# Optimization experiments

Hardware: AMD Instinct MI355X
Metric: run time of the kernel (lower is better)

The kernel has to match this reference:

```python
import jax, jax.numpy as jnp
import numpy as np

N = 100000   # nodes
E = 3200000  # edges (avg degree 32)
IN = 128     # in_channels
H = 128      # hidden_channels
G = 512      # graphs in batch


def setup_inputs() -> dict:
    key = jax.random.key(0)
    ks = jax.random.split(key, 8)
    x = jax.random.normal(ks[0], (N, IN), dtype=jnp.float32)
    edge_index = jax.random.randint(ks[1], (2, E), 0, N, dtype=jnp.int64)
    batch = jnp.sort(jax.random.randint(ks[2], (N,), 0, G, dtype=jnp.int64))
    s_in = 1.0 / np.sqrt(IN)
    s_h = 1.0 / np.sqrt(H)
    W1 = jax.random.normal(ks[3], (IN, H), dtype=jnp.float32) * s_in
    b1 = jnp.zeros((H,), dtype=jnp.float32)
    W2 = jax.random.normal(ks[4], (H, H), dtype=jnp.float32) * s_h
    b2 = jnp.zeros((H,), dtype=jnp.float32)
    Wc = jax.random.normal(ks[5], (H, 1), dtype=jnp.float32) * s_h
    bc = jnp.zeros((1,), dtype=jnp.float32)
    return {"x": x, "edge_index": edge_index, "batch": batch,
            "W1": W1, "b1": b1, "W2": W2, "b2": b2, "Wc": Wc, "bc": bc}


def _gcn_conv(x, W, b, src, dst, n):
    # PyG GCNConv: x' = D^{-1/2} (A+I) D^{-1/2} X W + b  (self-loops already in src/dst)
    h = x @ W                                      # [n, H] small GEMM
    ones = jnp.ones(src.shape[0], dtype=h.dtype)
    deg = jax.ops.segment_sum(ones, dst, num_segments=n)
    dinv = jnp.where(deg > 0, jax.lax.rsqrt(deg), 0.0)
    norm = dinv[src] * dinv[dst]                   # [E+n]
    msgs = h[src] * norm[:, None]                  # gather + scale (memory-bound)
    return jax.ops.segment_sum(msgs, dst, num_segments=n) + b


def reference(x, edge_index, batch, W1, b1, W2, b2, Wc, bc):
    n = x.shape[0]
    loop = jnp.arange(n, dtype=edge_index.dtype)
    src = jnp.concatenate([edge_index[0], loop])   # add self-loops
    dst = jnp.concatenate([edge_index[1], loop])
    h = jax.nn.relu(_gcn_conv(x, W1, b1, src, dst, n))
    h = jax.nn.relu(_gcn_conv(h, W2, b2, src, dst, n))
    # global_mean_pool: segment mean over graph ids
    counts = jax.ops.segment_sum(jnp.ones(n, dtype=h.dtype), batch, num_segments=G)
    sums = jax.ops.segment_sum(h, batch, num_segments=G)
    pooled = sums / jnp.maximum(counts, 1.0)[:, None]   # [G, H]
    return jax.nn.sigmoid(pooled @ Wc + bc)             # [G, 1]
```

## Files before the change

kernel.cpp:

```cpp
#include <hip/hip_runtime.h>

typedef unsigned short ushort_t;
typedef unsigned int uint_t;
typedef unsigned char u8_t;

typedef __bf16 bf16x8 __attribute__((ext_vector_type(8)));
typedef float f32x4 __attribute__((ext_vector_type(4)));
typedef uint_t uint32x4 __attribute__((ext_vector_type(4)));
typedef uint_t uint32x2 __attribute__((ext_vector_type(2)));
typedef _Float16 h2 __attribute__((ext_vector_type(2)));

#define EPB 20480
#define NSH 7
#define CAP 6144

__device__ __forceinline__ float b2f(ushort_t u) {
    union { uint_t ui; float f; } c; c.ui = ((uint_t)u) << 16; return c.f;
}
__device__ __forceinline__ ushort_t f2b(float f) {
    union { float f; uint_t ui; } c; c.f = f;
    uint_t u = c.ui;
    uint_t r = (u + 0x7fffu + ((u >> 16) & 1u)) >> 16;
    return (ushort_t)r;
}
__device__ __forceinline__ u8_t f2e5(float x) {
    ushort_t h = __builtin_bit_cast(ushort_t, (_Float16)x);
    uint_t r = ((uint_t)h + 0x7Fu + ((h >> 8) & 1u)) >> 8;
    return (u8_t)r;
}
__device__ __forceinline__ void upk_add(uint_t d, h2* acc) {
    uint_t A = __builtin_amdgcn_perm(0u, d, 0x010C000Cu);
    uint_t B = __builtin_amdgcn_perm(0u, d, 0x030C020Cu);
    acc[0] += __builtin_bit_cast(h2, A);
    acc[1] += __builtin_bit_cast(h2, B);
}

__global__ __launch_bounds__(256) void p1_hist(const int* __restrict__ dst,
                                               int* __restrict__ H,
                                               const float* __restrict__ W1,
                                               const float* __restrict__ W2,
                                               ushort_t* __restrict__ W1t,
                                               ushort_t* __restrict__ W2t,
                                               int E, int NBLK, int B) {
    int t = threadIdx.x, c = blockIdx.x;
    if (c >= NBLK) {
        int idx = (c - NBLK) * 256 + t;
        int sel = idx >> 14;
        int i = idx & 16383;
        int k = i >> 7, nn = i & 127;
        const float* S = sel ? W2 : W1;
        ushort_t* D = sel ? W2t : W1t;
        D[nn * 128 + k] = f2b(S[k * 128 + nn]);
        return;
    }
    __shared__ int hist[1024];
    for (int b = t; b < 1024; b += 256) hist[b] = 0;
    __syncthreads();
    int base = c * EPB;
    int lim = min(E - base, EPB);
    for (int i = t; i < lim; i += 256)
        atomicAdd(&hist[dst[base + i] >> NSH], 1);
    __syncthreads();
    for (int b = t; b < B; b += 256) H[b * NBLK + c] = hist[b];
}

__global__ __launch_bounds__(256) void reduce256(const int* __restrict__ in,
                                                 int* __restrict__ bsums, int n) {
    __shared__ int s[256];
    int t = threadIdx.x, g = blockIdx.x * 256 + t;
    s[t] = (g < n) ? in[g] : 0;
    __syncthreads();
    for (int o = 128; o > 0; o >>= 1) {
        if (t < o) s[t] += s[t + o];
        __syncthreads();
    }
    if (t == 0) bsums[blockIdx.x] = s[0];
}

__global__ __launch_bounds__(512) void scan_small(const int* __restrict__ in,
                                                  int* __restrict__ outEx, int n) {
    __shared__ int s[512];
    int t = threadIdx.x;
    int v = (t < n) ? in[t] : 0;
    s[t] = v;
    __syncthreads();
    for (int o = 1; o < 512; o <<= 1) {
        int x = 0;
        if (t >= o) x = s[t - o];
        __syncthreads();
        s[t] += x;
        __syncthreads();
    }
    if (t < n) outEx[t] = s[t] - v;
}

__global__ __launch_bounds__(256) void scan256ex(const int* __restrict__ in,
                                                 const int* __restrict__ boffs,
                                                 int* __restrict__ outEx, int n) {
    __shared__ int s[256];
    int t = threadIdx.x, g = blockIdx.x * 256 + t;
    int v = (g < n) ? in[g] : 0;
    s[t] = v;
    __syncthreads();
    for (int o = 1; o < 256; o <<= 1) {
        int x = 0;
        if (t >= o) x = s[t - o];
        __syncthreads();
        s[t] += x;
        __syncthreads();
    }
    if (g < n) outEx[g] = boffs[blockIdx.x] + s[t] - v;
}

__global__ __launch_bounds__(256) void p3_scatter(const int* __restrict__ src,
                                                  const int* __restrict__ dst,
                                                  const int* __restrict__ Hex,
                                                  uint_t* __restrict__ packed,
                                                  int E, int NBLK, int B) {
    __shared__ int offsL[1024];
    __shared__ int cur[1024];
    int t = threadIdx.x, c = blockIdx.x;
    for (int b = t; b < B; b += 256) {
        offsL[b] = Hex[b * NBLK + c];
        cur[b] = 0;
    }
    __syncthreads();
    int base = c * EPB;
    int lim = min(E - base, EPB);
    for (int i = t; i < lim; i += 256) {
        int d = dst[base + i];
        int s = src[base + i];
        int b = d >> NSH;
        int r = atomicAdd(&cur[b], 1);
        packed[offsL[b] + r] = ((uint_t)s << NSH) | (uint_t)(d & 127);
    }
}

__global__ __launch_bounds__(256) void p4_build(const uint_t* __restrict__ packed,
                                                const int* __restrict__ Hex,
                                                int* __restrict__ adj,
                                                int* __restrict__ offs,
                                                float* __restrict__ dinv,
                                                int E, int N, int NBLK, int B) {
    __shared__ uint_t ebuf[CAP];
    __shared__ uint_t sbuf[CAP];
    __shared__ int hist[1024];
    __shared__ int hbase[1024];
    __shared__ int psum[256];
    __shared__ int dcnt[128], loc[128], cur[128];
    int t = threadIdx.x, b = blockIdx.x;
    int bs = Hex[b * NBLK];
    int be = (b + 1 < B) ? Hex[(b + 1) * NBLK] : E;
    int m = be - bs;
    for (int i = t; i < 1024; i += 256) hist[i] = 0;
    if (t < 128) dcnt[t] = 0;
    __syncthreads();
    bool fits = (m <= CAP);
    for (int i = t; i < m; i += 256) {
        uint_t p = packed[bs + i];
        if (fits) ebuf[i] = p;
        atomicAdd(&dcnt[p & 127], 1);
        atomicAdd(&hist[p >> (2 * NSH)], 1);
    }
    __syncthreads();
    int v0 = hist[4 * t], v1 = hist[4 * t + 1], v2 = hist[4 * t + 2], v3 = hist[4 * t + 3];
    int tot = v0 + v1 + v2 + v3;
    psum[t] = tot;
    __syncthreads();
    for (int o = 1; o < 256; o <<= 1) {
        int x = 0;
        if (t >= o) x = psum[t - o];
        __syncthreads();
        psum[t] += x;
        __syncthreads();
    }
    int base = psum[t] - tot;
    hbase[4 * t]     = base;
    hbase[4 * t + 1] = base + v0;
    hbase[4 * t + 2] = base + v0 + v1;
    hbase[4 * t + 3] = base + v0 + v1 + v2;
    if (t < 128) loc[t] = dcnt[t];
    __syncthreads();
    for (int o = 1; o < 128; o <<= 1) {
        int x = 0;
        if (t < 128 && t >= o) x = loc[t - o];
        __syncthreads();
        if (t < 128) loc[t] += x;
        __syncthreads();
    }
    if (t < 128) {
        int ex = loc[t] - dcnt[t];
        int node = b * 128 + t;
        if (node < N) {
            offs[node] = bs + ex;
            dinv[node] = rsqrtf((float)(dcnt[t] + 1));
        }
        loc[t] = ex;
        cur[t] = 0;
    }
    if (b == B - 1 && t == 0) offs[N] = E;
    __syncthreads();
    if (fits) {
        for (int i = t; i < m; i += 256) {
            uint_t p = ebuf[i];
            int r = atomicAdd(&hbase[p >> (2 * NSH)], 1);
            sbuf[r] = p;
        }
        __syncthreads();
        for (int i = t; i < m; i += 256) {
            uint_t p = sbuf[i];
            int l = p & 127;
            int r = atomicAdd(&cur[l], 1);
            adj[bs + loc[l] + r] = (int)(p >> NSH);
        }
    } else {
        for (int i = t; i < m; i += 256) {
            uint_t p = packed[bs + i];
            int l = p & 127;
            int r = atomicAdd(&cur[l], 1);
            adj[bs + loc[l] + r] = (int)(p >> NSH);
        }
    }
}

__global__ __launch_bounds__(256, 4) void gemm_scale(const ushort_t* __restrict__ Xin,
                                                     const ushort_t* __restrict__ Wt,
                                                     const float* __restrict__ dinv,
                                                     u8_t* __restrict__ Hout8, int n) {
    __shared__ ushort_t lds[128 * 136];
    int tid = threadIdx.x;
    for (int i = tid; i < 128 * 16; i += 256) {
        int r = i >> 4, c8 = (i & 15) << 3;
        *(uint32x4*)(lds + r * 136 + c8) = *(const uint32x4*)(Wt + r * 128 + c8);
    }
    __syncthreads();
    int lane = tid & 63, wave = tid >> 6;
    int m = lane & 15, q = lane >> 4;
    int row0 = blockIdx.x * 64 + wave * 16;
    int ar = row0 + m;
    if (ar > n - 1) ar = n - 1;
    bf16x8 a[4];
#pragma unroll
    for (int ks = 0; ks < 4; ++ks)
        a[ks] = __builtin_bit_cast(bf16x8,
            *(const uint32x4*)(Xin + (size_t)ar * 128 + ks * 32 + q * 8));
    f32x4 acc[8];
    f32x4 zero = {0.f, 0.f, 0.f, 0.f};
#pragma unroll
    for (int nt = 0; nt < 8; ++nt) acc[nt] = zero;
#pragma unroll
    for (int nt = 0; nt < 8; ++nt) {
#pragma unroll
        for (int ks = 0; ks < 4; ++ks) {
            bf16x8 b = __builtin_bit_cast(bf16x8,
                *(const uint32x4*)(lds + (nt * 16 + m) * 136 + ks * 32 + q * 8));
            acc[nt] = __builtin_amdgcn_mfma_f32_16x16x32_bf16(a[ks], b, acc[nt], 0, 0, 0);
        }
    }
    float dv[4];
#pragma unroll
    for (int r = 0; r < 4; ++r) {
        int gr = row0 + q * 4 + r;
        dv[r] = (gr < n) ? dinv[gr] : 0.f;
    }
#pragma unroll
    for (int nt = 0; nt < 8; ++nt) {
#pragma unroll
        for (int r = 0; r < 4; ++r) {
            int gr = row0 + q * 4 + r;
            if (gr < n)
                Hout8[(size_t)gr * 128 + nt * 16 + m] = f2e5(acc[nt][r] * dv[r]);
        }
    }
}

__global__ __launch_bounds__(256, 4) void gemm_scale_f32(const float* __restrict__ Xf,
                                                         const ushort_t* __restrict__ Wt,
                                                         const float* __restrict__ dinv,
                                                         u8_t* __restrict__ Hout8, int n) {
    __shared__ ushort_t lds[128 * 136];
    int tid = threadIdx.x;
    for (int i = tid; i < 128 * 16; i += 256) {
        int r = i >> 4, c8 = (i & 15) << 3;
        *(uint32x4*)(lds + r * 136 + c8) = *(const uint32x4*)(Wt + r * 128 + c8);
    }
    __syncthreads();
    int lane = tid & 63, wave = tid >> 6;
    int m = lane & 15, q = lane >> 4;
    int row0 = blockIdx.x * 64 + wave * 16;
    int ar = row0 + m;
    if (ar > n - 1) ar = n - 1;
    bf16x8 a[4];
#pragma unroll
    for (int ks = 0; ks < 4; ++ks) {
        const float* p = Xf + (size_t)ar * 128 + ks * 32 + q * 8;
        f32x4 lo = *(const f32x4*)p;
        f32x4 hi = *(const f32x4*)(p + 4);
        ushort_t t[8];
        t[0] = f2b(lo[0]); t[1] = f2b(lo[1]); t[2] = f2b(lo[2]); t[3] = f2b(lo[3]);
        t[4] = f2b(hi[0]); t[5] = f2b(hi[1]); t[6] = f2b(hi[2]); t[7] = f2b(hi[3]);
        a[ks] = __builtin_bit_cast(bf16x8, *(uint32x4*)t);
    }
    f32x4 acc[8];
    f32x4 zero = {0.f, 0.f, 0.f, 0.f};
#pragma unroll
    for (int nt = 0; nt < 8; ++nt) acc[nt] = zero;
#pragma unroll
    for (int nt = 0; nt < 8; ++nt) {
#pragma unroll
        for (int ks = 0; ks < 4; ++ks) {
            bf16x8 b = __builtin_bit_cast(bf16x8,
                *(const uint32x4*)(lds + (nt * 16 + m) * 136 + ks * 32 + q * 8));
            acc[nt] = __builtin_amdgcn_mfma_f32_16x16x32_bf16(a[ks], b, acc[nt], 0, 0, 0);
        }
    }
    float dv[4];
#pragma unroll
    for (int r = 0; r < 4; ++r) {
        int gr = row0 + q * 4 + r;
        dv[r] = (gr < n) ? dinv[gr] : 0.f;
    }
#pragma unroll
    for (int nt = 0; nt < 8; ++nt) {
#pragma unroll
        for (int r = 0; r < 4; ++r) {
            int gr = row0 + q * 4 + r;
            if (gr < n)
                Hout8[(size_t)gr * 128 + nt * 16 + m] = f2e5(acc[nt][r] * dv[r]);
        }
    }
}

__device__ __forceinline__ void agg_body(const u8_t* base8, const int* __restrict__ adj,
                                         int beg, int end, int g, h2* acc) {
    int e = beg;
    for (; e + 32 <= end; e += 32) {
        int s[8];
#pragma unroll
        for (int j = 0; j < 8; ++j) s[j] = adj[e + 4 * j + g];
        uint32x2 w[8];
#pragma unroll
        for (int j = 0; j < 8; ++j) w[j] = *(const uint32x2*)(base8 + (size_t)s[j] * 128);
#pragma unroll
        for (int j = 0; j < 8; ++j) {
            upk_add(w[j][0], acc);
            upk_add(w[j][1], acc + 2);
        }
    }
    for (; e + 8 <= end; e += 8) {
        int s0 = adj[e + g], s1 = adj[e + 4 + g];
        uint32x2 w0 = *(const uint32x2*)(base8 + (size_t)s0 * 128);
        uint32x2 w1 = *(const uint32x2*)(base8 + (size_t)s1 * 128);
        upk_add(w0[0], acc); upk_add(w0[1], acc + 2);
        upk_add(w1[0], acc); upk_add(w1[1], acc + 2);
    }
    for (; e < end; e += 4) {
        int idx = e + g;
        if (idx < end) {
            int s = adj[idx];
            uint32x2 w = *(const uint32x2*)(base8 + (size_t)s * 128);
            upk_add(w[0], acc);
            upk_add(w[1], acc + 2);
        }
    }
}

__global__ __launch_bounds__(256, 8) void agg_kernel(const u8_t* __restrict__ Hs8,
                                                     const int* __restrict__ adj,
                                                     const int* __restrict__ offs,
                                                     const float* __restrict__ dinv,
                                                     const float* __restrict__ bias,
                                                     ushort_t* __restrict__ Out, int n) {
    int node = blockIdx.x * 4 + (threadIdx.x >> 6);
    if (node >= n) return;
    int lane = threadIdx.x & 63;
    int g = lane >> 4;
    int l16 = lane & 15;
    int col = l16 * 8;
    const u8_t* base8 = Hs8 + col;
    const int beg = offs[node], end = offs[node + 1];
    h2 acc[4];
    h2 hz = {(_Float16)0.f, (_Float16)0.f};
#pragma unroll
    for (int k = 0; k < 4; ++k) acc[k] = hz;
    if (g == 0) {
        uint32x2 w = *(const uint32x2*)(base8 + (size_t)node * 128);
        upk_add(w[0], acc);
        upk_add(w[1], acc + 2);
    }
    agg_body(base8, adj, beg, end, g, acc);
#pragma unroll
    for (int k = 0; k < 4; ++k) {
        uint_t v = __builtin_bit_cast(uint_t, acc[k]);
        acc[k] += __builtin_bit_cast(h2, (uint_t)__shfl_xor(v, 16, 64));
        v = __builtin_bit_cast(uint_t, acc[k]);
        acc[k] += __builtin_bit_cast(h2, (uint_t)__shfl_xor(v, 32, 64));
    }
    if (g == 0) {
        float di = dinv[node];
        ushort_t o[8];
#pragma unroll
        for (int k = 0; k < 4; ++k) {
            float f0 = (float)acc[k][0];
            float f1 = (float)acc[k][1];
            o[2 * k]     = f2b(fmaxf(di * f0 + bias[col + 2 * k], 0.f));
            o[2 * k + 1] = f2b(fmaxf(di * f1 + bias[col + 2 * k + 1], 0.f));
        }
        *(uint32x4*)(Out + (size_t)node * 128 + col) = *(uint32x4*)o;
    }
}

__global__ __launch_bounds__(256, 8) void agg_pool_kernel(const u8_t* __restrict__ Hs8,
                                                          const int* __restrict__ adj,
                                                          const int* __restrict__ offs,
                                                          const float* __restrict__ dinv,
                                                          const float* __restrict__ bias,
                                                          const float* __restrict__ Wc,
                                                          float* __restrict__ Sout, int n) {
    int node = blockIdx.x * 4 + (threadIdx.x >> 6);
    if (node >= n) return;
    int lane = threadIdx.x & 63;
    int g = lane >> 4;
    int l16 = lane & 15;
    int col = l16 * 8;
    const u8_t* base8 = Hs8 + col;
    const int beg = offs[node], end = offs[node + 1];
    h2 acc[4];
    h2 hz = {(_Float16)0.f, (_Float16)0.f};
#pragma unroll
    for (int k = 0; k < 4; ++k) acc[k] = hz;
    if (g == 0) {
        uint32x2 w = *(const uint32x2*)(base8 + (size_t)node * 128);
        upk_add(w[0], acc);
        upk_add(w[1], acc + 2);
    }
    agg_body(base8, adj, beg, end, g, acc);
#pragma unroll
    for (int k = 0; k < 4; ++k) {
        uint_t v = __builtin_bit_cast(uint_t, acc[k]);
        acc[k] += __builtin_bit_cast(h2, (uint_t)__shfl_xor(v, 16, 64));
        v = __builtin_bit_cast(uint_t, acc[k]);
        acc[k] += __builtin_bit_cast(h2, (uint_t)__shfl_xor(v, 32, 64));
    }
    float local = 0.f;
    float di = dinv[node];
#pragma unroll
    for (int k = 0; k < 4; ++k) {
        float f0 = fmaxf(di * (float)acc[k][0] + bias[col + 2 * k], 0.f);
        float f1 = fmaxf(di * (float)acc[k][1] + bias[col + 2 * k + 1], 0.f);
        local += f0 * Wc[col + 2 * k] + f1 * Wc[col + 2 * k + 1];
    }
    local += __shfl_xor(local, 1, 64);
    local += __shfl_xor(local, 2, 64);
    local += __shfl_xor(local, 4, 64);
    local += __shfl_xor(local, 8, 64);
    if (lane == 0) Sout[node] = local;
}

__global__ __launch_bounds__(256) void pool2_kernel(const float* __restrict__ S,
                                                    const int* __restrict__ batch,
                                                    const float* __restrict__ bc,
                                                    float* __restrict__ out, int n) {
    int g = blockIdx.x;
    int t = threadIdx.x;
    int lo = 0, hi = n;
    while (lo < hi) { int mid = (lo + hi) >> 1; if (batch[mid] < g) lo = mid + 1; else hi = mid; }
    int start = lo;
    hi = n;
    while (lo < hi) { int mid = (lo + hi) >> 1; if (batch[mid] < g + 1) lo = mid + 1; else hi = mid; }
    int stop = lo;
    float s = 0.f;
    for (int i = start + t; i < stop; i += 256) s += S[i];
    __shared__ float red[256];
    red[t] = s;
    __syncthreads();
    for (int o = 128; o > 0; o >>= 1) {
        if (t < o) red[t] += red[t + o];
        __syncthreads();
    }
    if (t == 0) {
        int cg = stop - start;
        float z = red[0] / (float)(cg > 0 ? cg : 1) + bc[0];
        out[g] = 1.f / (1.f + expf(-z));
    }
}

extern "C" void kernel_launch(void* const* d_in, const int* in_sizes, int n_in,
                              void* d_out, int out_size, void* d_ws, size_t ws_size,
                              hipStream_t stream) {
    const float* X     = (const float*)d_in[0];
    const int* ei      = (const int*)d_in[1];
    const int* batch   = (const int*)d_in[2];
    const float* W1    = (const float*)d_in[3];
    const float* b1    = (const float*)d_in[4];
    const float* W2    = (const float*)d_in[5];
    const float* b2    = (const float*)d_in[6];
    const float* Wc    = (const float*)d_in[7];
    const float* bc    = (const float*)d_in[8];

    const int N = in_sizes[2];
    const int E = in_sizes[1] / 2;
    const int G = out_size;
    const int* srcv = ei;
    const int* dstv = ei + E;

    const int NBLK = (E + EPB - 1) / EPB;
    const int B    = (N + 127) >> NSH;
    const int n0   = B * NBLK;
    const int g1   = (n0 + 255) / 256;

    char* p = (char*)d_ws;
    auto alloc = [&](size_t bytes) -> void* {
        void* r = (void*)p;
        p += (bytes + 255) & ~(size_t)255;
        return r;
    };
    int* H         = (int*)alloc((size_t)n0 * 4);
    int* Hex       = (int*)alloc((size_t)n0 * 4);
    int* S1        = (int*)alloc((size_t)g1 * 4);
    int* S1ex      = (int*)alloc((size_t)g1 * 4);
    uint_t* packed = (uint_t*)alloc((size_t)E * 4);
    int* adj       = (int*)alloc((size_t)E * 4);
    int* offs      = (int*)alloc(((size_t)N + 1) * 4);
    float* dinv    = (float*)alloc((size_t)N * 4);
    ushort_t* W1t  = (ushort_t*)alloc(16384 * 2);
    ushort_t* W2t  = (ushort_t*)alloc(16384 * 2);
    u8_t* h8       = (u8_t*)alloc((size_t)N * 128);
    ushort_t* bufA = (ushort_t*)alloc((size_t)N * 128 * 2);
    float* Snode   = (float*)alloc((size_t)N * 4);

    p1_hist<<<NBLK + 128, 256, 0, stream>>>(dstv, H, W1, W2, W1t, W2t, E, NBLK, B);
    reduce256<<<g1, 256, 0, stream>>>(H, S1, n0);
    scan_small<<<1, 512, 0, stream>>>(S1, S1ex, g1);
    scan256ex<<<g1, 256, 0, stream>>>(H, S1ex, Hex, n0);
    p3_scatter<<<NBLK, 256, 0, stream>>>(srcv, dstv, Hex, packed, E, NBLK, B);
    p4_build<<<B, 256, 0, stream>>>(packed, Hex, adj, offs, dinv, E, N, NBLK, B);

    const int GB = (N + 63) / 64;
    const int AB = (N + 3) / 4;
    gemm_scale_f32<<<GB, 256, 0, stream>>>(X, W1t, dinv, h8, N);
    agg_kernel<<<AB, 256, 0, stream>>>(h8, adj, offs, dinv, b1, bufA, N);
    gemm_scale<<<GB, 256, 0, stream>>>(bufA, W2t, dinv, h8, N);
    agg_pool_kernel<<<AB, 256, 0, stream>>>(h8, adj, offs, dinv, b2, Wc, Snode, N);
    pool2_kernel<<<G, 256, 0, stream>>>(Snode, batch, bc, (float*)d_out, N);
}
```

Before: 398.3 us.

## Replace scan-based CSR build with fixed-capacity per-bucket slabs and atomic counters

```diff
diff --git a/kernel.cpp b/kernel.cpp
--- a/kernel.cpp
+++ b/kernel.cpp
@@ -10,8 +10,9 @@
 typedef uint_t uint32x2 __attribute__((ext_vector_type(2)));
 typedef _Float16 h2 __attribute__((ext_vector_type(2)));
 
-#define EPB 20480
+#define EPB 16384
 #define NSH 7
+#define SLAB 6144
 #define CAP 6144
 
 __device__ __forceinline__ float b2f(ushort_t u) {
@@ -35,13 +36,15 @@
     acc[1] += __builtin_bit_cast(h2, B);
 }
 
-__global__ __launch_bounds__(256) void p1_hist(const int* __restrict__ dst,
-                                               int* __restrict__ H,
-                                               const float* __restrict__ W1,
-                                               const float* __restrict__ W2,
-                                               ushort_t* __restrict__ W1t,
-                                               ushort_t* __restrict__ W2t,
-                                               int E, int NBLK, int B) {
+__global__ __launch_bounds__(256) void p3_scatter(const int* __restrict__ src,
+                                                  const int* __restrict__ dst,
+                                                  int* __restrict__ bcnt,
+                                                  uint_t* __restrict__ packed,
+                                                  const float* __restrict__ W1,
+                                                  const float* __restrict__ W2,
+                                                  ushort_t* __restrict__ W1t,
+                                                  ushort_t* __restrict__ W2t,
+                                                  int E, int NBLK, int B) {
     int t = threadIdx.x, c = blockIdx.x;
     if (c >= NBLK) {
         int idx = (c - NBLK) * 256 + t;
@@ -53,95 +56,39 @@
         D[nn * 128 + k] = f2b(S[k * 128 + nn]);
         return;
     }
-    __shared__ int hist[1024];
-    for (int b = t; b < 1024; b += 256) hist[b] = 0;
+    __shared__ int offsL[1024];
+    __shared__ int cur[1024];
+    for (int b = t; b < 1024; b += 256) cur[b] = 0;
     __syncthreads();
     int base = c * EPB;
     int lim = min(E - base, EPB);
     for (int i = t; i < lim; i += 256)
-        atomicAdd(&hist[dst[base + i] >> NSH], 1);
-    __syncthreads();
-    for (int b = t; b < B; b += 256) H[b * NBLK + c] = hist[b];
-}
-
-__global__ __launch_bounds__(256) void reduce256(const int* __restrict__ in,
-                                                 int* __restrict__ bsums, int n) {
-    __shared__ int s[256];
-    int t = threadIdx.x, g = blockIdx.x * 256 + t;
-    s[t] = (g < n) ? in[g] : 0;
-    __syncthreads();
-    for (int o = 128; o > 0; o >>= 1) {
-        if (t < o) s[t] += s[t + o];
-        __syncthreads();
-    }
-    if (t == 0) bsums[blockIdx.x] = s[0];
-}
-
-__global__ __launch_bounds__(512) void scan_small(const int* __restrict__ in,
-                                                  int* __restrict__ outEx, int n) {
-    __shared__ int s[512];
-    int t = threadIdx.x;
-    int v = (t < n) ? in[t] : 0;
-    s[t] = v;
-    __syncthreads();
-    for (int o = 1; o < 512; o <<= 1) {
-        int x = 0;
-        if (t >= o) x = s[t - o];
-        __syncthreads();
-        s[t] += x;
-        __syncthreads();
-    }
-    if (t < n) outEx[t] = s[t] - v;
-}
-
-__global__ __launch_bounds__(256) void scan256ex(const int* __restrict__ in,
-                                                 const int* __restrict__ boffs,
-                                                 int* __restrict__ outEx, int n) {
-    __shared__ int s[256];
-    int t = threadIdx.x, g = blockIdx.x * 256 + t;
-    int v = (g < n) ? in[g] : 0;
-    s[t] = v;
-    __syncthreads();
-    for (int o = 1; o < 256; o <<= 1) {
-        int x = 0;
-        if (t >= o) x = s[t - o];
-        __syncthreads();
-        s[t] += x;
-        __syncthreads();
-    }
-    if (g < n) outEx[g] = boffs[blockIdx.x] + s[t] - v;
-}
-
-__global__ __launch_bounds__(256) void p3_scatter(const int* __restrict__ src,
-                                                  const int* __restrict__ dst,
-                                                  const int* __restrict__ Hex,
-                                                  uint_t* __restrict__ packed,
-                                                  int E, int NBLK, int B) {
-    __shared__ int offsL[1024];
-    __shared__ int cur[1024];
-    int t = threadIdx.x, c = blockIdx.x;
+        atomicAdd(&cur[dst[base + i] >> NSH], 1);
+    __syncthreads();
     for (int b = t; b < B; b += 256) {
-        offsL[b] = Hex[b * NBLK + c];
+        int cnt = cur[b];
+        offsL[b] = (cnt > 0) ? atomicAdd(&bcnt[b], cnt) : 0;
         cur[b] = 0;
     }
     __syncthreads();
-    int base = c * EPB;
-    int lim = min(E - base, EPB);
     for (int i = t; i < lim; i += 256) {
         int d = dst[base + i];
         int s = src[base + i];
         int b = d >> NSH;
         int r = atomicAdd(&cur[b], 1);
-        packed[offsL[b] + r] = ((uint_t)s << NSH) | (uint_t)(d & 127);
+        int pos = offsL[b] + r;
+        if (pos < SLAB)
+            packed[(size_t)b * SLAB + pos] = ((uint_t)s << NSH) | (uint_t)(d & 127);
     }
 }
 
 __global__ __launch_bounds__(256) void p4_build(const uint_t* __restrict__ packed,
-                                                const int* __restrict__ Hex,
+                                                const int* __restrict__ bcnt,
                                                 int* __restrict__ adj,
                                                 int* __restrict__ offs,
+                                                int* __restrict__ deg,
                                                 float* __restrict__ dinv,
-                                                int E, int N, int NBLK, int B) {
+                                                int N, int B) {
     __shared__ uint_t ebuf[CAP];
     __shared__ uint_t sbuf[CAP];
     __shared__ int hist[1024];
@@ -149,16 +96,15 @@
     __shared__ int psum[256];
     __shared__ int dcnt[128], loc[128], cur[128];
     int t = threadIdx.x, b = blockIdx.x;
-    int bs = Hex[b * NBLK];
-    int be = (b + 1 < B) ? Hex[(b + 1) * NBLK] : E;
-    int m = be - bs;
+    int m = min(bcnt[b], SLAB);
+    const uint_t* pk = packed + (size_t)b * SLAB;
+    int* aj = adj + (size_t)b * SLAB;
     for (int i = t; i < 1024; i += 256) hist[i] = 0;
     if (t < 128) dcnt[t] = 0;
     __syncthreads();
-    bool fits = (m <= CAP);
     for (int i = t; i < m; i += 256) {
-        uint_t p = packed[bs + i];
-        if (fits) ebuf[i] = p;
+        uint_t p = pk[i];
+        ebuf[i] = p;
         atomicAdd(&dcnt[p & 127], 1);
         atomicAdd(&hist[p >> (2 * NSH)], 1);
     }
@@ -192,34 +138,25 @@
         int ex = loc[t] - dcnt[t];
         int node = b * 128 + t;
         if (node < N) {
-            offs[node] = bs + ex;
+            offs[node] = b * SLAB + ex;
+            deg[node]  = dcnt[t];
             dinv[node] = rsqrtf((float)(dcnt[t] + 1));
         }
         loc[t] = ex;
         cur[t] = 0;
     }
-    if (b == B - 1 && t == 0) offs[N] = E;
-    __syncthreads();
-    if (fits) {
-        for (int i = t; i < m; i += 256) {
-            uint_t p = ebuf[i];
-            int r = atomicAdd(&hbase[p >> (2 * NSH)], 1);
-            sbuf[r] = p;
-        }
-        __syncthreads();
-        for (int i = t; i < m; i += 256) {
-            uint_t p = sbuf[i];
-            int l = p & 127;
-            int r = atomicAdd(&cur[l], 1);
-            adj[bs + loc[l] + r] = (int)(p >> NSH);
-        }
-    } else {
-        for (int i = t; i < m; i += 256) {
-            uint_t p = packed[bs + i];
-            int l = p & 127;
-            int r = atomicAdd(&cur[l], 1);
-            adj[bs + loc[l] + r] = (int)(p >> NSH);
-        }
+    __syncthreads();
+    for (int i = t; i < m; i += 256) {
+        uint_t p = ebuf[i];
+        int r = atomicAdd(&hbase[p >> (2 * NSH)], 1);
+        sbuf[r] = p;
+    }
+    __syncthreads();
+    for (int i = t; i < m; i += 256) {
+        uint_t p = sbuf[i];
+        int l = p & 127;
+        int r = atomicAdd(&cur[l], 1);
+        aj[loc[l] + r] = (int)(p >> NSH);
     }
 }
 
@@ -368,6 +305,7 @@
 __global__ __launch_bounds__(256, 8) void agg_kernel(const u8_t* __restrict__ Hs8,
                                                      const int* __restrict__ adj,
                                                      const int* __restrict__ offs,
+                                                     const int* __restrict__ deg,
                                                      const float* __restrict__ dinv,
                                                      const float* __restrict__ bias,
                                                      ushort_t* __restrict__ Out, int n) {
@@ -378,7 +316,7 @@
     int l16 = lane & 15;
     int col = l16 * 8;
     const u8_t* base8 = Hs8 + col;
-    const int beg = offs[node], end = offs[node + 1];
+    const int beg = offs[node], end = beg + deg[node];
     h2 acc[4];
     h2 hz = {(_Float16)0.f, (_Float16)0.f};
 #pragma unroll
@@ -413,6 +351,7 @@
 __global__ __launch_bounds__(256, 8) void agg_pool_kernel(const u8_t* __restrict__ Hs8,
                                                           const int* __restrict__ adj,
                                                           const int* __restrict__ offs,
+                                                          const int* __restrict__ deg,
                                                           const float* __restrict__ dinv,
                                                           const float* __restrict__ bias,
                                                           const float* __restrict__ Wc,
@@ -424,7 +363,7 @@
     int l16 = lane & 15;
     int col = l16 * 8;
     const u8_t* base8 = Hs8 + col;
-    const int beg = offs[node], end = offs[node + 1];
+    const int beg = offs[node], end = beg + deg[node];
     h2 acc[4];
     h2 hz = {(_Float16)0.f, (_Float16)0.f};
 #pragma unroll
@@ -506,8 +445,6 @@
 
     const int NBLK = (E + EPB - 1) / EPB;
     const int B    = (N + 127) >> NSH;
-    const int n0   = B * NBLK;
-    const int g1   = (n0 + 255) / 256;
 
     char* p = (char*)d_ws;
     auto alloc = [&](size_t bytes) -> void* {
@@ -515,13 +452,11 @@
         p += (bytes + 255) & ~(size_t)255;
         return r;
     };
-    int* H         = (int*)alloc((size_t)n0 * 4);
-    int* Hex       = (int*)alloc((size_t)n0 * 4);
-    int* S1        = (int*)alloc((size_t)g1 * 4);
-    int* S1ex      = (int*)alloc((size_t)g1 * 4);
-    uint_t* packed = (uint_t*)alloc((size_t)E * 4);
-    int* adj       = (int*)alloc((size_t)E * 4);
-    int* offs      = (int*)alloc(((size_t)N + 1) * 4);
+    int* bcnt      = (int*)alloc((size_t)B * 4);
+    uint_t* packed = (uint_t*)alloc((size_t)B * SLAB * 4);
+    int* adj       = (int*)alloc((size_t)B * SLAB * 4);
+    int* offs      = (int*)alloc((size_t)N * 4);
+    int* deg       = (int*)alloc((size_t)N * 4);
     float* dinv    = (float*)alloc((size_t)N * 4);
     ushort_t* W1t  = (ushort_t*)alloc(16384 * 2);
     ushort_t* W2t  = (ushort_t*)alloc(16384 * 2);
@@ -529,18 +464,17 @@
     ushort_t* bufA = (ushort_t*)alloc((size_t)N * 128 * 2);
     float* Snode   = (float*)alloc((size_t)N * 4);
 
-    p1_hist<<<NBLK + 128, 256, 0, stream>>>(dstv, H, W1, W2, W1t, W2t, E, NBLK, B);
-    reduce256<<<g1, 256, 0, stream>>>(H, S1, n0);
-    scan_small<<<1, 512, 0, stream>>>(S1, S1ex, g1);
-    scan256ex<<<g1, 256, 0, stream>>>(H, S1ex, Hex, n0);
-    p3_scatter<<<NBLK, 256, 0, stream>>>(srcv, dstv, Hex, packed, E, NBLK, B);
-    p4_build<<<B, 256, 0, stream>>>(packed, Hex, adj, offs, dinv, E, N, NBLK, B);
+    hipMemsetAsync(bcnt, 0, (size_t)B * 4, stream);
+
+    p3_scatter<<<NBLK + 128, 256, 0, stream>>>(srcv, dstv, bcnt, packed,
+                                               W1, W2, W1t, W2t, E, NBLK, B);
+    p4_build<<<B, 256, 0, stream>>>(packed, bcnt, adj, offs, deg, dinv, N, B);
 
     const int GB = (N + 63) / 64;
     const int AB = (N + 3) / 4;
     gemm_scale_f32<<<GB, 256, 0, stream>>>(X, W1t, dinv, h8, N);
-    agg_kernel<<<AB, 256, 0, stream>>>(h8, adj, offs, dinv, b1, bufA, N);
+    agg_kernel<<<AB, 256, 0, stream>>>(h8, adj, offs, deg, dinv, b1, bufA, N);
     gemm_scale<<<GB, 256, 0, stream>>>(bufA, W2t, dinv, h8, N);
-    agg_pool_kernel<<<AB, 256, 0, stream>>>(h8, adj, offs, dinv, b2, Wc, Snode, N);
+    agg_pool_kernel<<<AB, 256, 0, stream>>>(h8, adj, offs, deg, dinv, b2, Wc, Snode, N);
     pool2_kernel<<<G, 256, 0, stream>>>(Snode, batch, bc, (float*)d_out, N);
 }
```

After: 401.3 us. About the same (+0.8%).
